# Optimization experiments

Measured on AMD Instinct MI355X. Metric: run time of the kernel, lower is better.

The kernel has to match this reference:

```python
import jax, jax.numpy as jnp
import numpy as np

ALPHA = 0.75      # normalized min-sum scaling factor
MAX_ITER = 50     # fixed number of BP iterations (original loops until convergence or max_iter)
B, M, N, DEG = 64, 8192, 16384, 8


def setup_inputs() -> dict:
    key = jax.random.key(0)
    k1, k2, k3 = jax.random.split(key, 3)
    llr0 = jax.random.normal(k1, (B, N), dtype=jnp.float32)
    synd = jax.random.randint(k2, (B, M), 0, 2, dtype=jnp.int32)
    # variable-node column indices per check node; value == N marks a dummy (padded) edge
    V_c_col = jax.random.randint(k3, (M, DEG), 0, N + 1, dtype=jnp.int32)
    return {"llr0": llr0, "synd": synd, "V_c_col": V_c_col}


def _decode(llr0, synd, V_c_col):
    b_sz, n_var = llr0.shape
    m_chk, deg = V_c_col.shape
    dt = llr0.dtype
    # u_init: prior LLRs extended with a dummy +inf column (index n_var)
    u_init = jnp.concatenate([llr0, jnp.full((b_sz, 1), jnp.inf, dt)], axis=1)  # [B, N+1]
    mask_dummy = (V_c_col == n_var)                                             # [M, deg]
    sgn_s = (1.0 - 2.0 * synd.astype(dt))[:, :, None]                           # [B, M, 1], (-1)^syndrome
    flat_cols = V_c_col.reshape(-1)

    def cn_update(a):
        # normalized min-sum check-node update with extrinsic (leave-one-out) sign and min
        mag = jnp.abs(a)
        sgn = jnp.sign(a)
        sgn = jnp.where(sgn == 0, jnp.ones((), dt), sgn)
        prod_sgn = jnp.prod(sgn, axis=-1, keepdims=True)
        sgn_ex = prod_sgn * sgn                      # divide == multiply for +-1 signs
        m1 = jnp.min(mag, axis=-1, keepdims=True)
        idx = jnp.argmin(mag, axis=-1)
        onehot = jax.nn.one_hot(idx, deg, dtype=jnp.bool_)
        m2 = jnp.min(jnp.where(onehot, jnp.inf, mag), axis=-1, keepdims=True)
        mag_ex = jnp.where(onehot, m2, m1)           # min excluding self edge
        return ALPHA * sgn_s * sgn_ex * mag_ex

    def llr_update(b_c2v):
        # scatter-add check->variable messages over column indices
        contrib = jax.vmap(
            lambda bb: jax.ops.segment_sum(bb.reshape(-1), flat_cols, num_segments=n_var + 1)
        )(b_c2v)
        return u_init + contrib

    def step(carry, i):
        msg, l_v = carry
        first = (i == 0)
        # variable->check: extrinsic LLR gather (first iteration uses the prior directly)
        a_v2c = jnp.where(first, u_init[:, V_c_col], l_v[:, V_c_col] - msg)
        b_c2v = cn_update(a_v2c)
        b_c2v = jnp.where(mask_dummy[None], jnp.zeros((), dt), b_c2v)
        l_v = llr_update(b_c2v)
        return (b_c2v, l_v), None

    msg0 = jnp.zeros((b_sz, m_chk, deg), dt)
    l_v0 = jnp.zeros((b_sz, n_var + 1), dt)
    (_, l_v), _ = jax.lax.scan(jax.checkpoint(step), (msg0, l_v0), jnp.arange(MAX_ITER))
    return l_v  # posterior LLRs, [B, N+1] (last column is the dummy)


def reference(llr0, synd, V_c_col):
    return _decode(llr0, synd, V_c_col)
```

## Files before the change

### kernel.cpp

```cpp
#include <hip/hip_runtime.h>
#include <hip/hip_fp16.h>
#include <math.h>


constexpr int B_ = 64;
constexpr int M_ = 8192;
constexpr int N_ = 16384;
constexpr int ITER_ = 50;
constexpr int NV_ = N_ + 1;
constexpr int NVB_ = NV_ * B_;
constexpr int NVB16_ = NVB_ / 8;
constexpr int SB_ = M_ * B_;
constexpr float ALPHA_ = 0.75f;

__global__ __launch_bounds__(256) void setup_u(const float* __restrict__ llr0,
                                               __half* __restrict__ u_h,
                                               __half* __restrict__ lv0,
                                               __half* __restrict__ lv1,
                                               __half* __restrict__ lv2) {
    __shared__ float t[64][65];
    const int tid = threadIdx.x, lane = tid & 63, r4 = tid >> 6;
    const int nb = blockIdx.x;
    if (nb < 256) {
        #pragma unroll
        for (int r = r4; r < 64; r += 4)
            t[lane][r] = llr0[(size_t)r * N_ + nb * 64 + lane];
        __syncthreads();
        #pragma unroll
        for (int r = r4; r < 64; r += 4) {
            __half v = __float2half(t[r][lane]);
            int idx = (nb * 64 + r) * B_ + lane;
            u_h[idx] = v; lv0[idx] = v; lv1[idx] = v;
        }
    } else {
        if (tid < 64) {
            int idx = N_ * B_ + tid;
            __half inf = __ushort_as_half((unsigned short)0x7C00);
            u_h[idx] = inf; lv0[idx] = inf; lv1[idx] = inf; lv2[idx] = inf;
        }
    }
}

__global__ __launch_bounds__(256) void setup_st(const int* __restrict__ synd,
                                                uint2* __restrict__ st) {
    __shared__ int t[64][65];
    const int tid = threadIdx.x, lane = tid & 63, r4 = tid >> 6;
    const int mb = blockIdx.x;
    #pragma unroll
    for (int r = r4; r < 64; r += 4)
        t[lane][r] = synd[(size_t)r * M_ + mb * 64 + lane];
    __syncthreads();
    #pragma unroll
    for (int r = r4; r < 64; r += 4) {
        unsigned s = (unsigned)t[r][lane] & 1u;
        st[(mb * 64 + r) * B_ + lane] = make_uint2(0u, s << 11);
    }
}

__device__ __forceinline__ void process_check(const int* __restrict__ c,
                                              uint2 s,
                                              const __half* __restrict__ g,
                                              __half* __restrict__ lvS,
                                              uint2* __restrict__ stw,
                                              int lane) {
    const __half2 f12 = *reinterpret_cast<const __half2*>(&s.x);
    const float f1 = __low2float(f12), f2 = __high2float(f12);
    const unsigned pk = s.y;
    const unsigned negI = pk & 255u, amI = (pk >> 8) & 7u;
    const unsigned synd = (pk >> 11) & 1u, baseI = (pk >> 12) & 1u;

    float a[8];
    #pragma unroll
    for (int d = 0; d < 8; ++d) {
        float mag = (d == (int)amI) ? f2 : f1;
        float msg = ((baseI ^ (negI >> d)) & 1u) ? -mag : mag;
        a[d] = __half2float(g[d]) - msg;
    }

    float m1 = __builtin_inff(), m2 = __builtin_inff();
    int amin = 0;
    unsigned negbits = 0;
    #pragma unroll
    for (int d = 0; d < 8; ++d) {
        float mag = fabsf(a[d]);
        negbits |= (unsigned)(a[d] < 0.f) << d;
        if (mag < m1) { m2 = m1; m1 = mag; amin = d; }
        else if (mag < m2) { m2 = mag; }
    }
    const unsigned base = (__popc(negbits) & 1u) ^ synd;
    const float f1n = ALPHA_ * m1;
    const float f2n = ALPHA_ * m2;

    const __half2 nh = __halves2half2(__float2half(f1n), __float2half(f2n));
    uint2 o;
    o.x = *reinterpret_cast<const unsigned*>(&nh);
    o.y = negbits | ((unsigned)amin << 8) | (synd << 11) | (base << 12);
    *stw = o;

    #pragma unroll
    for (int d = 0; d < 8; ++d) {
        float v = (d == amin) ? f2n : f1n;
        float t = ((base ^ (negbits >> d)) & 1u) ? -v : v;
        float p = __shfl_xor(t, 1);
        if (c[d] != N_ && (lane & 1) == 0) {
            __half2 h2 = __halves2half2(__float2half(t), __float2half(p));
            unsafeAtomicAdd(reinterpret_cast<__half2*>(lvS + (size_t)c[d] * B_ + lane), h2);
        }
    }
}

__global__ __launch_bounds__(256, 4) void bp_iter(const int* __restrict__ cols,
                                                  const __half* __restrict__ u_h,
                                                  const __half* __restrict__ lvG,
                                                  __half* __restrict__ lvS,
                                                  __half* __restrict__ lvI,
                                                  uint2* __restrict__ st) {
    const int tid = threadIdx.x;
    const int gid = blockIdx.x * 256 + tid;

    if (gid < NVB16_) {
        reinterpret_cast<uint4*>(lvI)[gid] =
            reinterpret_cast<const uint4*>(u_h)[gid];
    }

    const int lane = tid & 63;
    const int w = blockIdx.x * 4 + (tid >> 6);
    const int mA = w, mB = w + 4096;
    const int siA = mA * B_ + lane, siB = mB * B_ + lane;

    const int4* pA = reinterpret_cast<const int4*>(cols + mA * 8);
    const int4* pB = reinterpret_cast<const int4*>(cols + mB * 8);
    int4 a0 = pA[0], a1 = pA[1], b0 = pB[0], b1 = pB[1];
    uint2 sA = st[siA], sB = st[siB];

    int cA[8] = {a0.x, a0.y, a0.z, a0.w, a1.x, a1.y, a1.z, a1.w};
    int cB[8] = {b0.x, b0.y, b0.z, b0.w, b1.x, b1.y, b1.z, b1.w};

    __half gA[8], gB[8];
    #pragma unroll
    for (int d = 0; d < 8; ++d) gA[d] = lvG[(size_t)cA[d] * B_ + lane];
    #pragma unroll
    for (int d = 0; d < 8; ++d) gB[d] = lvG[(size_t)cB[d] * B_ + lane];

    process_check(cA, sA, gA, lvS, st + siA, lane);
    process_check(cB, sB, gB, lvS, st + siB, lane);
}

__global__ __launch_bounds__(256) void out_t(const __half* __restrict__ lv,
                                             float* __restrict__ out) {
    __shared__ float t[64][65];
    const int tid = threadIdx.x, lane = tid & 63, r4 = tid >> 6;
    const int nb = blockIdx.x;
    if (nb < 256) {
        #pragma unroll
        for (int r = r4; r < 64; r += 4)
            t[r][lane] = __half2float(lv[(nb * 64 + r) * B_ + lane]);
        __syncthreads();
        #pragma unroll
        for (int r = r4; r < 64; r += 4)
            out[(size_t)r * NV_ + nb * 64 + lane] = t[lane][r];
    } else {
        if (tid < 64)
            out[(size_t)tid * NV_ + N_] = 0.0f;
    }
}

extern "C" void kernel_launch(void* const* d_in, const int* in_sizes, int n_in,
                              void* d_out, int out_size, void* d_ws, size_t ws_size,
                              hipStream_t stream) {
    const float* llr0 = (const float*)d_in[0];
    const int* synd   = (const int*)d_in[1];
    const int* colsp  = (const int*)d_in[2];
    float* out = (float*)d_out;

    __half* ws = (__half*)d_ws;
    __half* u_h = ws;
    __half* lv0 = u_h + NVB_;
    __half* lv1 = lv0 + NVB_;
    __half* lv2 = lv1 + NVB_;
    uint2* st = (uint2*)(lv2 + NVB_);
    __half* lv[3] = {lv0, lv1, lv2};

    hipLaunchKernelGGL(setup_u, dim3(257), dim3(256), 0, stream, llr0, u_h, lv0, lv1, lv2);
    hipLaunchKernelGGL(setup_st, dim3(128), dim3(256), 0, stream, synd, st);

    for (int i = 0; i < ITER_; ++i) {
        hipLaunchKernelGGL(bp_iter, dim3(1024), dim3(256), 0, stream,
                           colsp, u_h, lv[i % 3], lv[(i + 1) % 3], lv[(i + 2) % 3], st);
    }

    hipLaunchKernelGGL(out_t, dim3(257), dim3(256), 0, stream, lv[ITER_ % 3], out);
}
```

Before: 616.5 us.

## Split batch into 8-wide slices and remap check waves to slice layout

Relayouts the LLR buffers and the check state from a [N+1][64 batch] interleave into 8 slices of [N+1][8 batch]. Each wave now handles 8 checks times 8 batches of one slice, and the grid doubles to cover all slices. The goal is a smaller per-slice working set for the random gathers and atomic adds, which should help cache locality. The cost is that each gather and atomic now touches a 16-byte segment per column instead of a contiguous 128-byte row, which may fragment memory transactions.

```diff
diff --git a/kernel.cpp b/kernel.cpp
--- a/kernel.cpp
+++ b/kernel.cpp
@@ -8,9 +8,10 @@
 constexpr int N_ = 16384;
 constexpr int ITER_ = 50;
 constexpr int NV_ = N_ + 1;
-constexpr int NVB_ = NV_ * B_;
-constexpr int NVB16_ = NVB_ / 8;
-constexpr int SB_ = M_ * B_;
+constexpr int SHB_ = 8;
+constexpr int SSTRIDE_ = NV_ * SHB_;
+constexpr int NVB_ = SSTRIDE_ * 8;
+constexpr int SU4_ = SSTRIDE_ / 8;
 constexpr float ALPHA_ = 0.75f;
 
 __global__ __launch_bounds__(256) void setup_u(const float* __restrict__ llr0,
@@ -24,19 +25,25 @@
     if (nb < 256) {
         #pragma unroll
         for (int r = r4; r < 64; r += 4)
-            t[lane][r] = llr0[(size_t)r * N_ + nb * 64 + lane];
+            t[r][lane] = llr0[(size_t)r * N_ + nb * 64 + lane];
         __syncthreads();
         #pragma unroll
-        for (int r = r4; r < 64; r += 4) {
-            __half v = __float2half(t[r][lane]);
-            int idx = (nb * 64 + r) * B_ + lane;
-            u_h[idx] = v; lv0[idx] = v; lv1[idx] = v;
+        for (int k = 0; k < 2; ++k) {
+            const int idx = k * 256 + tid;
+            const int nl = idx >> 3, bl = idx & 7;
+            #pragma unroll
+            for (int s = 0; s < 8; ++s) {
+                __half v = __float2half(t[s * 8 + bl][nl]);
+                const int a = s * SSTRIDE_ + (nb * 64 + nl) * 8 + bl;
+                u_h[a] = v; lv0[a] = v; lv1[a] = v;
+            }
         }
     } else {
         if (tid < 64) {
-            int idx = N_ * B_ + tid;
+            const int s = tid >> 3, b = tid & 7;
+            const int a = s * SSTRIDE_ + N_ * 8 + b;
             __half inf = __ushort_as_half((unsigned short)0x7C00);
-            u_h[idx] = inf; lv0[idx] = inf; lv1[idx] = inf; lv2[idx] = inf;
+            u_h[a] = inf; lv0[a] = inf; lv1[a] = inf; lv2[a] = inf;
         }
     }
 }
@@ -48,64 +55,12 @@
     const int mb = blockIdx.x;
     #pragma unroll
     for (int r = r4; r < 64; r += 4)
-        t[lane][r] = synd[(size_t)r * M_ + mb * 64 + lane];
+        t[r][lane] = synd[(size_t)r * M_ + mb * 64 + lane];
     __syncthreads();
     #pragma unroll
     for (int r = r4; r < 64; r += 4) {
-        unsigned s = (unsigned)t[r][lane] & 1u;
-        st[(mb * 64 + r) * B_ + lane] = make_uint2(0u, s << 11);
-    }
-}
-
-__device__ __forceinline__ void process_check(const int* __restrict__ c,
-                                              uint2 s,
-                                              const __half* __restrict__ g,
-                                              __half* __restrict__ lvS,
-                                              uint2* __restrict__ stw,
-                                              int lane) {
-    const __half2 f12 = *reinterpret_cast<const __half2*>(&s.x);
-    const float f1 = __low2float(f12), f2 = __high2float(f12);
-    const unsigned pk = s.y;
-    const unsigned negI = pk & 255u, amI = (pk >> 8) & 7u;
-    const unsigned synd = (pk >> 11) & 1u, baseI = (pk >> 12) & 1u;
-
-    float a[8];
-    #pragma unroll
-    for (int d = 0; d < 8; ++d) {
-        float mag = (d == (int)amI) ? f2 : f1;
-        float msg = ((baseI ^ (negI >> d)) & 1u) ? -mag : mag;
-        a[d] = __half2float(g[d]) - msg;
-    }
-
-    float m1 = __builtin_inff(), m2 = __builtin_inff();
-    int amin = 0;
-    unsigned negbits = 0;
-    #pragma unroll
-    for (int d = 0; d < 8; ++d) {
-        float mag = fabsf(a[d]);
-        negbits |= (unsigned)(a[d] < 0.f) << d;
-        if (mag < m1) { m2 = m1; m1 = mag; amin = d; }
-        else if (mag < m2) { m2 = mag; }
-    }
-    const unsigned base = (__popc(negbits) & 1u) ^ synd;
-    const float f1n = ALPHA_ * m1;
-    const float f2n = ALPHA_ * m2;
-
-    const __half2 nh = __halves2half2(__float2half(f1n), __float2half(f2n));
-    uint2 o;
-    o.x = *reinterpret_cast<const unsigned*>(&nh);
-    o.y = negbits | ((unsigned)amin << 8) | (synd << 11) | (base << 12);
-    *stw = o;
-
-    #pragma unroll
-    for (int d = 0; d < 8; ++d) {
-        float v = (d == amin) ? f2n : f1n;
-        float t = ((base ^ (negbits >> d)) & 1u) ? -v : v;
-        float p = __shfl_xor(t, 1);
-        if (c[d] != N_ && (lane & 1) == 0) {
-            __half2 h2 = __halves2half2(__float2half(t), __float2half(p));
-            unsafeAtomicAdd(reinterpret_cast<__half2*>(lvS + (size_t)c[d] * B_ + lane), h2);
-        }
+        unsigned s = (unsigned)t[lane][r] & 1u;
+        st[(size_t)(mb * 64 + r) * 64 + lane] = make_uint2(0u, s << 11);
     }
 }
 
@@ -116,34 +71,80 @@
                                                   __half* __restrict__ lvI,
                                                   uint2* __restrict__ st) {
     const int tid = threadIdx.x;
-    const int gid = blockIdx.x * 256 + tid;
+    const int s = blockIdx.x & 7;
+    const int bs = blockIdx.x >> 3;
 
-    if (gid < NVB16_) {
-        reinterpret_cast<uint4*>(lvI)[gid] =
-            reinterpret_cast<const uint4*>(u_h)[gid];
+    {
+        const int idx = bs * 256 + tid;
+        if (idx < SU4_) {
+            reinterpret_cast<uint4*>(lvI + (size_t)s * SSTRIDE_)[idx] =
+                reinterpret_cast<const uint4*>(u_h + (size_t)s * SSTRIDE_)[idx];
+        }
     }
 
     const int lane = tid & 63;
-    const int w = blockIdx.x * 4 + (tid >> 6);
-    const int mA = w, mB = w + 4096;
-    const int siA = mA * B_ + lane, siB = mB * B_ + lane;
+    const int c = lane >> 3, b = lane & 7;
+    const int g = bs * 4 + (tid >> 6);
+    const int m = g * 8 + c;
 
-    const int4* pA = reinterpret_cast<const int4*>(cols + mA * 8);
-    const int4* pB = reinterpret_cast<const int4*>(cols + mB * 8);
-    int4 a0 = pA[0], a1 = pA[1], b0 = pB[0], b1 = pB[1];
-    uint2 sA = st[siA], sB = st[siB];
+    const __half* __restrict__ lvg = lvG + (size_t)s * SSTRIDE_;
+    __half* __restrict__ lvs = lvS + (size_t)s * SSTRIDE_;
 
-    int cA[8] = {a0.x, a0.y, a0.z, a0.w, a1.x, a1.y, a1.z, a1.w};
-    int cB[8] = {b0.x, b0.y, b0.z, b0.w, b1.x, b1.y, b1.z, b1.w};
+    const int4* cp = reinterpret_cast<const int4*>(cols + m * 8);
+    const int4 c0 = cp[0], c1 = cp[1];
+    const int cc[8] = {c0.x, c0.y, c0.z, c0.w, c1.x, c1.y, c1.z, c1.w};
 
-    __half gA[8], gB[8];
+    uint2* __restrict__ stp = st + (size_t)m * 64 + s * 8 + b;
+    const uint2 sv = *stp;
+
+    __half gg[8];
     #pragma unroll
-    for (int d = 0; d < 8; ++d) gA[d] = lvG[(size_t)cA[d] * B_ + lane];
+    for (int d = 0; d < 8; ++d) gg[d] = lvg[cc[d] * 8 + b];
+
+    const __half2 f12 = *reinterpret_cast<const __half2*>(&sv.x);
+    const float f1 = __low2float(f12), f2 = __high2float(f12);
+    const unsigned pk = sv.y;
+    const unsigned negI = pk & 255u, amI = (pk >> 8) & 7u;
+    const unsigned syn = (pk >> 11) & 1u, baseI = (pk >> 12) & 1u;
+
+    float a[8];
     #pragma unroll
-    for (int d = 0; d < 8; ++d) gB[d] = lvG[(size_t)cB[d] * B_ + lane];
+    for (int d = 0; d < 8; ++d) {
+        float mag = (d == (int)amI) ? f2 : f1;
+        float msg = ((baseI ^ (negI >> d)) & 1u) ? -mag : mag;
+        a[d] = __half2float(gg[d]) - msg;
+    }
 
-    process_check(cA, sA, gA, lvS, st + siA, lane);
-    process_check(cB, sB, gB, lvS, st + siB, lane);
+    float m1 = __builtin_inff(), m2 = __builtin_inff();
+    int am = 0;
+    unsigned nb = 0;
+    #pragma unroll
+    for (int d = 0; d < 8; ++d) {
+        float mag = fabsf(a[d]);
+        nb |= (unsigned)(a[d] < 0.f) << d;
+        if (mag < m1) { m2 = m1; m1 = mag; am = d; }
+        else if (mag < m2) { m2 = mag; }
+    }
+    const unsigned base = (__popc(nb) & 1u) ^ syn;
+    const float f1n = ALPHA_ * m1;
+    const float f2n = ALPHA_ * m2;
+
+    const __half2 nh = __halves2half2(__float2half(f1n), __float2half(f2n));
+    uint2 o;
+    o.x = *reinterpret_cast<const unsigned*>(&nh);
+    o.y = nb | ((unsigned)am << 8) | (syn << 11) | (base << 12);
+    *stp = o;
+
+    #pragma unroll
+    for (int d = 0; d < 8; ++d) {
+        float v = (d == am) ? f2n : f1n;
+        float t = ((base ^ (nb >> d)) & 1u) ? -v : v;
+        float p = __shfl_xor(t, 1);
+        if (cc[d] != N_ && (b & 1) == 0) {
+            __half2 h2 = __halves2half2(__float2half(t), __float2half(p));
+            unsafeAtomicAdd(reinterpret_cast<__half2*>(lvs + cc[d] * 8 + b), h2);
+        }
+    }
 }
 
 __global__ __launch_bounds__(256) void out_t(const __half* __restrict__ lv,
@@ -154,7 +155,8 @@
     if (nb < 256) {
         #pragma unroll
         for (int r = r4; r < 64; r += 4)
-            t[r][lane] = __half2float(lv[(nb * 64 + r) * B_ + lane]);
+            t[r][lane] = __half2float(
+                lv[(lane >> 3) * SSTRIDE_ + (nb * 64 + r) * 8 + (lane & 7)]);
         __syncthreads();
         #pragma unroll
         for (int r = r4; r < 64; r += 4)
@@ -185,7 +187,7 @@
     hipLaunchKernelGGL(setup_st, dim3(128), dim3(256), 0, stream, synd, st);
 
     for (int i = 0; i < ITER_; ++i) {
-        hipLaunchKernelGGL(bp_iter, dim3(1024), dim3(256), 0, stream,
+        hipLaunchKernelGGL(bp_iter, dim3(2048), dim3(256), 0, stream,
                            colsp, u_h, lv[i % 3], lv[(i + 1) % 3], lv[(i + 2) % 3], st);
     }
 
```

Result: slower. 1.614 ms (+161.7%).
